# Kernel tuning notes

Hardware: AMD Instinct MI355X
Metric: run time of the kernel (lower is better)

Reference implementation:

```python
import jax, jax.numpy as jnp
import numpy as np

S = 30.0
M = 0.5
EPS = 1e-07


def setup_inputs() -> dict:
    key = jax.random.key(0)
    k1, k2, k3 = jax.random.split(key, 3)
    B, D, C = 1024, 512, 100000
    embeddings = jax.random.normal(k1, (B, D), dtype=jnp.float32)
    # xavier_uniform for weight [C, D]
    limit = float(np.sqrt(6.0 / (C + D)))
    weight = jax.random.uniform(k2, (C, D), dtype=jnp.float32, minval=-limit, maxval=limit)
    labels = jax.random.randint(k3, (B,), 0, C, dtype=jnp.int64)
    return {"embeddings": embeddings, "weight": weight, "labels": labels}


def _l2norm(x, axis=-1):
    # matches F.normalize(p=2, eps=1e-12)
    n = jnp.linalg.norm(x, axis=axis, keepdims=True)
    return x / jnp.maximum(n, 1e-12)


def reference(embeddings, weight, labels):
    # cosine: [B, C] = normalized embeddings @ normalized weight^T
    cosine = _l2norm(embeddings) @ _l2norm(weight).T
    B = cosine.shape[0]
    rows = jnp.arange(B)
    # margin transform only on the target logit per row (same math as
    # one_hot combine: cos(acos(clamp(c)) + m) at the label column)
    tgt = cosine[rows, labels]
    theta = jnp.arccos(jnp.clip(tgt, -1.0 + EPS, 1.0 - EPS))
    target_logit = jnp.cos(theta + M)
    output = cosine.at[rows, labels].set(target_logit)
    return output * S
```

## Files before the change

### kernel.cpp

```cpp
#include <hip/hip_runtime.h>
#include <hip/hip_bf16.h>

typedef __attribute__((ext_vector_type(8))) short bf16x8;
typedef __attribute__((ext_vector_type(4))) float f32x4;

#define B_ROWS 1024
#define C_COLS 100000
#define K_DIM  512
#define SCALE_S 30.0f
#define MARGIN_M 0.5f
#define EPS_C 1e-7f

#define BM 256
#define BN 256
#define BK 64
#define NKT (K_DIM / BK)

__device__ __forceinline__ void gload_lds16(const __hip_bfloat16* g, __hip_bfloat16* l) {
    __builtin_amdgcn_global_load_lds((const __attribute__((address_space(1))) void*)g,
                                     (__attribute__((address_space(3))) void*)l,
                                     16, 0, 0);
}

__device__ __forceinline__ void barrier_fenced() {
    asm volatile("" ::: "memory");
    __builtin_amdgcn_s_barrier();
    asm volatile("" ::: "memory");
}

__global__ __launch_bounds__(256) void l2norm_bf16_rows(const float* __restrict__ in,
                                                        __hip_bfloat16* __restrict__ out,
                                                        int nrows) {
    int wid  = (int)((blockIdx.x * blockDim.x + threadIdx.x) >> 6);
    int lane = threadIdx.x & 63;
    if (wid >= nrows) return;
    const float4* rp = (const float4*)(in + (size_t)wid * K_DIM);
    float4 v0 = rp[lane];
    float4 v1 = rp[lane + 64];
    float ss = v0.x * v0.x + v0.y * v0.y + v0.z * v0.z + v0.w * v0.w
             + v1.x * v1.x + v1.y * v1.y + v1.z * v1.z + v1.w * v1.w;
#pragma unroll
    for (int off = 32; off > 0; off >>= 1) ss += __shfl_xor(ss, off, 64);
    float scale = 1.0f / fmaxf(sqrtf(ss), 1e-12f);
    union { __hip_bfloat16 h[4]; int2 q; } a, b;
    a.h[0] = __float2bfloat16(v0.x * scale);
    a.h[1] = __float2bfloat16(v0.y * scale);
    a.h[2] = __float2bfloat16(v0.z * scale);
    a.h[3] = __float2bfloat16(v0.w * scale);
    b.h[0] = __float2bfloat16(v1.x * scale);
    b.h[1] = __float2bfloat16(v1.y * scale);
    b.h[2] = __float2bfloat16(v1.z * scale);
    b.h[3] = __float2bfloat16(v1.w * scale);
    int2* op = (int2*)(out + (size_t)wid * K_DIM);
    op[lane]      = a.q;
    op[lane + 64] = b.q;
}

__global__ __launch_bounds__(512, 2) void arcface_gemm(
        const __hip_bfloat16* __restrict__ A,
        const __hip_bfloat16* __restrict__ W,
        float* __restrict__ out) {
    __shared__ __hip_bfloat16 sA[2 * 2 * 256 * 32];
    __shared__ __hip_bfloat16 sB[2 * 2 * 256 * 32];

    const int nwg = (int)gridDim.x;
    const int q8 = nwg >> 3, r8 = nwg & 7;
    const int xcd = (int)blockIdx.x & 7, ii = (int)blockIdx.x >> 3;
    const int wg = (xcd < r8 ? xcd * (q8 + 1) : r8 * (q8 + 1) + (xcd - r8) * q8) + ii;
    const int mt = wg & 3, nt = wg >> 2;
    const long m0 = (long)mt * BM;
    const long n0 = (long)nt * BN;

    const int tid  = (int)threadIdx.x;
    const int lane = tid & 63;
    const int w    = tid >> 6;
    const int wm   = w >> 2;
    const int wn   = w & 3;
    const int lidx = lane & 15, lk = lane >> 4;

    const int srow  = tid >> 2;
    const int sslot = (tid & 3) ^ (srow & 3);

#define STAGE_A(buf, kh, kt) do {                                                   \
        gload_lds16(A + (m0 + srow) * K_DIM + (kt) * BK + (kh) * 32 + sslot * 8,    \
                    &sA[((((buf) * 2 + (kh)) * 256) * 32) + (0 * 512 + tid) * 8]);  \
        gload_lds16(A + (m0 + 128 + srow) * K_DIM + (kt) * BK + (kh) * 32 + sslot * 8, \
                    &sA[((((buf) * 2 + (kh)) * 256) * 32) + (1 * 512 + tid) * 8]);  \
    } while (0)

#define STAGE_B(buf, kh, kt) do {                                                   \
        long r0 = n0 + srow;       if (r0 >= C_COLS) r0 = C_COLS - 1;               \
        long r1 = n0 + 128 + srow; if (r1 >= C_COLS) r1 = C_COLS - 1;               \
        gload_lds16(W + r0 * K_DIM + (kt) * BK + (kh) * 32 + sslot * 8,             \
                    &sB[((((buf) * 2 + (kh)) * 256) * 32) + (0 * 512 + tid) * 8]);  \
        gload_lds16(W + r1 * K_DIM + (kt) * BK + (kh) * 32 + sslot * 8,             \
                    &sB[((((buf) * 2 + (kh)) * 256) * 32) + (1 * 512 + tid) * 8]);  \
    } while (0)

#define LDA(dst, c, kh, mh) do {                                                    \
        _Pragma("unroll")                                                           \
        for (int i = 0; i < 4; ++i) {                                               \
            int row = wm * 128 + (mh) * 64 + i * 16 + lidx;                         \
            dst[i] = *(const bf16x8*)&sA[(((c) * 2 + (kh)) * 256 + row) * 32        \
                                         + ((lk ^ (lidx & 3)) * 8)];                \
        }                                                                           \
    } while (0)

#define LDB(dst, c, kh) do {                                                        \
        _Pragma("unroll")                                                           \
        for (int n = 0; n < 4; ++n) {                                               \
            int row = wn * 64 + n * 16 + lidx;                                      \
            dst[n] = *(const bf16x8*)&sB[(((c) * 2 + (kh)) * 256 + row) * 32        \
                                         + ((lk ^ (lidx & 3)) * 8)];                \
        }                                                                           \
    } while (0)

#define MFMA16(mh, av_, bv_) do {                                                   \
        __builtin_amdgcn_s_setprio(1);                                              \
        _Pragma("unroll")                                                           \
        for (int m = 0; m < 4; ++m)                                                 \
            _Pragma("unroll")                                                       \
            for (int n = 0; n < 4; ++n)                                             \
                acc[(mh) * 4 + m][n] = __builtin_amdgcn_mfma_f32_16x16x32_bf16(     \
                    av_[m], bv_[n], acc[(mh) * 4 + m][n], 0, 0, 0);                 \
        __builtin_amdgcn_s_setprio(0);                                              \
    } while (0)

#define WAIT_LGKM0() do { asm volatile("s_waitcnt lgkmcnt(0)" ::: "memory"); \
                          __builtin_amdgcn_sched_barrier(0); } while (0)
#define WAIT_VM4()   asm volatile("s_waitcnt vmcnt(4)" ::: "memory")
#define WAIT_VM0()   asm volatile("s_waitcnt vmcnt(0)" ::: "memory")

    f32x4 acc[8][4];
#pragma unroll
    for (int m = 0; m < 8; ++m)
#pragma unroll
        for (int n = 0; n < 4; ++n) acc[m][n] = (f32x4){0.f, 0.f, 0.f, 0.f};

    STAGE_A(0, 0, 0); STAGE_B(0, 0, 0);
    STAGE_A(0, 1, 0); STAGE_B(0, 1, 0);
    WAIT_VM4();
    barrier_fenced();

    bf16x8 av[4], bv[4];
    for (int t = 0; t < NKT - 1; ++t) {
        const int c = t & 1, nb = c ^ 1;
        LDA(av, c, 0, 0); LDB(bv, c, 0);
        STAGE_A(nb, 0, t + 1);
        barrier_fenced(); WAIT_LGKM0();
        MFMA16(0, av, bv);
        barrier_fenced();
        LDA(av, c, 0, 1);
        STAGE_B(nb, 0, t + 1);
        barrier_fenced(); WAIT_LGKM0();
        MFMA16(1, av, bv);
        WAIT_VM4();
        barrier_fenced();
        LDA(av, c, 1, 0); LDB(bv, c, 1);
        STAGE_A(nb, 1, t + 1);
        barrier_fenced(); WAIT_LGKM0();
        MFMA16(0, av, bv);
        barrier_fenced();
        LDA(av, c, 1, 1);
        STAGE_B(nb, 1, t + 1);
        barrier_fenced(); WAIT_LGKM0();
        MFMA16(1, av, bv);
        WAIT_VM4();
        barrier_fenced();
    }
    {
        const int c = (NKT - 1) & 1;
        LDA(av, c, 0, 0); LDB(bv, c, 0);
        barrier_fenced(); WAIT_LGKM0();
        MFMA16(0, av, bv);
        barrier_fenced();
        LDA(av, c, 0, 1);
        barrier_fenced(); WAIT_LGKM0();
        MFMA16(1, av, bv);
        WAIT_VM0();
        barrier_fenced();
        LDA(av, c, 1, 0); LDB(bv, c, 1);
        barrier_fenced(); WAIT_LGKM0();
        MFMA16(0, av, bv);
        barrier_fenced();
        LDA(av, c, 1, 1);
        barrier_fenced(); WAIT_LGKM0();
        MFMA16(1, av, bv);
    }

    const long colb = n0 + wn * 64 + lidx;
#pragma unroll
    for (int mf = 0; mf < 8; ++mf) {
        long rowb = m0 + wm * 128 + mf * 16 + lk * 4;
#pragma unroll
        for (int nf = 0; nf < 4; ++nf) {
            long gc = colb + nf * 16;
            if (gc < C_COLS) {
#pragma unroll
                for (int j = 0; j < 4; ++j)
                    out[(rowb + j) * (long)C_COLS + gc] = acc[mf][nf][j] * SCALE_S;
            }
        }
    }
#undef STAGE_A
#undef STAGE_B
#undef LDA
#undef LDB
#undef MFMA16
#undef WAIT_LGKM0
#undef WAIT_VM4
#undef WAIT_VM0
}

__global__ void margin_fixup(float* __restrict__ out, const int* __restrict__ labels,
                             int nrows) {
    int b = blockIdx.x * blockDim.x + threadIdx.x;
    if (b >= nrows) return;
    int lab = labels[b];
    size_t idx = (size_t)b * C_COLS + (size_t)lab;
    float c = out[idx] * (1.0f / SCALE_S);
    c = fminf(fmaxf(c, -1.0f + EPS_C), 1.0f - EPS_C);
    float t = acosf(c) + MARGIN_M;
    out[idx] = cosf(t) * SCALE_S;
}

extern "C" void kernel_launch(void* const* d_in, const int* in_sizes, int n_in,
                              void* d_out, int out_size, void* d_ws, size_t ws_size,
                              hipStream_t stream) {
    const float* emb = (const float*)d_in[0];
    const float* wgt = (const float*)d_in[1];
    const int* labels = (const int*)d_in[2];
    float* out = (float*)d_out;

    __hip_bfloat16* embb = (__hip_bfloat16*)d_ws;
    __hip_bfloat16* wgtb = (__hip_bfloat16*)((char*)d_ws + (size_t)B_ROWS * K_DIM * 2);

    l2norm_bf16_rows<<<B_ROWS / 4, 256, 0, stream>>>(emb, embb, B_ROWS);
    l2norm_bf16_rows<<<C_COLS / 4, 256, 0, stream>>>(wgt, wgtb, C_COLS);

    const int ntiles = (C_COLS + BN - 1) / BN;
    arcface_gemm<<<4 * ntiles, 512, 0, stream>>>(embb, wgtb, out);

    margin_fixup<<<(B_ROWS + 255) / 256, 256, 0, stream>>>(out, labels, B_ROWS);
}
```

Before: 703.6 us.

## Make GEMM persistent with XCD-strided tiles, cross-tile prefetch, and vectorized transposed stores

Replaces the one-workgroup-per-tile grid with a persistent grid of 256 workgroups. Each workgroup loops over tiles strided by 32 within its XCD's column group and prefetches the next tile's first K-slab during the current tile's epilogue. The MFMA operands are swapped so each lane holds four consecutive columns, which allows float4 stores instead of scalar strided stores. The aim is to cut launch and tail overhead, overlap loads with the output write, and widen store transactions. In exchange it adds loop bookkeeping and may load-balance less evenly across workgroups.

```diff
diff --git a/kernel.cpp b/kernel.cpp
--- a/kernel.cpp
+++ b/kernel.cpp
@@ -15,6 +15,7 @@
 #define BN 256
 #define BK 64
 #define NKT (K_DIM / BK)
+#define N_TILES ((C_COLS + BN - 1) / BN)
 
 __device__ __forceinline__ void gload_lds16(const __hip_bfloat16* g, __hip_bfloat16* l) {
     __builtin_amdgcn_global_load_lds((const __attribute__((address_space(1))) void*)g,
@@ -63,13 +64,10 @@
     __shared__ __hip_bfloat16 sA[2 * 2 * 256 * 32];
     __shared__ __hip_bfloat16 sB[2 * 2 * 256 * 32];
 
-    const int nwg = (int)gridDim.x;
-    const int q8 = nwg >> 3, r8 = nwg & 7;
-    const int xcd = (int)blockIdx.x & 7, ii = (int)blockIdx.x >> 3;
-    const int wg = (xcd < r8 ? xcd * (q8 + 1) : r8 * (q8 + 1) + (xcd - r8) * q8) + ii;
-    const int mt = wg & 3, nt = wg >> 2;
-    const long m0 = (long)mt * BM;
-    const long n0 = (long)nt * BN;
+    const int x = (int)blockIdx.x & 7;
+    const int s = (int)blockIdx.x >> 3;
+    const int cnt = (x < (N_TILES & 7)) ? (N_TILES / 8 + 1) : (N_TILES / 8);
+    const int tot = 4 * cnt;
 
     const int tid  = (int)threadIdx.x;
     const int lane = tid & 63;
@@ -80,6 +78,9 @@
 
     const int srow  = tid >> 2;
     const int sslot = (tid & 3) ^ (srow & 3);
+
+#define TILE_MN(j) do { m0 = (long)((j) & 3) * BM;                                  \
+                        n0 = (long)(x + 8 * ((j) >> 2)) * BN; } while (0)
 
 #define STAGE_A(buf, kh, kt) do {                                                   \
         gload_lds16(A + (m0 + srow) * K_DIM + (kt) * BK + (kh) * 32 + sslot * 8,    \
@@ -97,6 +98,9 @@
                     &sB[((((buf) * 2 + (kh)) * 256) * 32) + (1 * 512 + tid) * 8]);  \
     } while (0)
 
+#define STAGE_FULL() do { STAGE_A(0, 0, 0); STAGE_B(0, 0, 0);                       \
+                          STAGE_A(0, 1, 0); STAGE_B(0, 1, 0); } while (0)
+
 #define LDA(dst, c, kh, mh) do {                                                    \
         _Pragma("unroll")                                                           \
         for (int i = 0; i < 4; ++i) {                                               \
@@ -122,7 +126,7 @@
             _Pragma("unroll")                                                       \
             for (int n = 0; n < 4; ++n)                                             \
                 acc[(mh) * 4 + m][n] = __builtin_amdgcn_mfma_f32_16x16x32_bf16(     \
-                    av_[m], bv_[n], acc[(mh) * 4 + m][n], 0, 0, 0);                 \
+                    bv_[n], av_[m], acc[(mh) * 4 + m][n], 0, 0, 0);                 \
         __builtin_amdgcn_s_setprio(0);                                              \
     } while (0)
 
@@ -132,78 +136,91 @@
 #define WAIT_VM0()   asm volatile("s_waitcnt vmcnt(0)" ::: "memory")
 
     f32x4 acc[8][4];
-#pragma unroll
-    for (int m = 0; m < 8; ++m)
-#pragma unroll
-        for (int n = 0; n < 4; ++n) acc[m][n] = (f32x4){0.f, 0.f, 0.f, 0.f};
-
-    STAGE_A(0, 0, 0); STAGE_B(0, 0, 0);
-    STAGE_A(0, 1, 0); STAGE_B(0, 1, 0);
-    WAIT_VM4();
-    barrier_fenced();
-
     bf16x8 av[4], bv[4];
-    for (int t = 0; t < NKT - 1; ++t) {
-        const int c = t & 1, nb = c ^ 1;
-        LDA(av, c, 0, 0); LDB(bv, c, 0);
-        STAGE_A(nb, 0, t + 1);
-        barrier_fenced(); WAIT_LGKM0();
-        MFMA16(0, av, bv);
-        barrier_fenced();
-        LDA(av, c, 0, 1);
-        STAGE_B(nb, 0, t + 1);
-        barrier_fenced(); WAIT_LGKM0();
-        MFMA16(1, av, bv);
+    long m0, n0;
+
+    TILE_MN(s);
+    STAGE_FULL();
+
+    for (int j = s; j < tot; j += 32) {
         WAIT_VM4();
         barrier_fenced();
-        LDA(av, c, 1, 0); LDB(bv, c, 1);
-        STAGE_A(nb, 1, t + 1);
-        barrier_fenced(); WAIT_LGKM0();
-        MFMA16(0, av, bv);
-        barrier_fenced();
-        LDA(av, c, 1, 1);
-        STAGE_B(nb, 1, t + 1);
-        barrier_fenced(); WAIT_LGKM0();
-        MFMA16(1, av, bv);
-        WAIT_VM4();
-        barrier_fenced();
+#pragma unroll
+        for (int m = 0; m < 8; ++m)
+#pragma unroll
+            for (int n = 0; n < 4; ++n) acc[m][n] = (f32x4){0.f, 0.f, 0.f, 0.f};
+
+        for (int t = 0; t < NKT - 1; ++t) {
+            const int c = t & 1, nb = c ^ 1;
+            LDA(av, c, 0, 0); LDB(bv, c, 0);
+            STAGE_A(nb, 0, t + 1);
+            barrier_fenced(); WAIT_LGKM0();
+            MFMA16(0, av, bv);
+            barrier_fenced();
+            LDA(av, c, 0, 1);
+            STAGE_B(nb, 0, t + 1);
+            barrier_fenced(); WAIT_LGKM0();
+            MFMA16(1, av, bv);
+            WAIT_VM4();
+            barrier_fenced();
+            LDA(av, c, 1, 0); LDB(bv, c, 1);
+            STAGE_A(nb, 1, t + 1);
+            barrier_fenced(); WAIT_LGKM0();
+            MFMA16(0, av, bv);
+            barrier_fenced();
+            LDA(av, c, 1, 1);
+            STAGE_B(nb, 1, t + 1);
+            barrier_fenced(); WAIT_LGKM0();
+            MFMA16(1, av, bv);
+            WAIT_VM4();
+            barrier_fenced();
+        }
+        {
+            const int c = (NKT - 1) & 1;
+            LDA(av, c, 0, 0); LDB(bv, c, 0);
+            barrier_fenced(); WAIT_LGKM0();
+            MFMA16(0, av, bv);
+            barrier_fenced();
+            LDA(av, c, 0, 1);
+            barrier_fenced(); WAIT_LGKM0();
+            MFMA16(1, av, bv);
+            WAIT_VM0();
+            barrier_fenced();
+            LDA(av, c, 1, 0); LDB(bv, c, 1);
+            barrier_fenced(); WAIT_LGKM0();
+            MFMA16(0, av, bv);
+            barrier_fenced();
+            LDA(av, c, 1, 1);
+            barrier_fenced(); WAIT_LGKM0();
+            MFMA16(1, av, bv);
+        }
+
+        {
+            const long cb = n0 + wn * 64 + lk * 4;
+#pragma unroll
+            for (int mf = 0; mf < 8; ++mf) {
+                float* orow = out + (m0 + wm * 128 + mf * 16 + lidx) * (long)C_COLS;
+#pragma unroll
+                for (int nf = 0; nf < 4; ++nf) {
+                    long c0 = cb + nf * 16;
+                    if (c0 < C_COLS) {
+                        float4 st = { acc[mf][nf][0] * SCALE_S, acc[mf][nf][1] * SCALE_S,
+                                      acc[mf][nf][2] * SCALE_S, acc[mf][nf][3] * SCALE_S };
+                        *(float4*)(orow + c0) = st;
+                    }
+                }
+            }
+        }
+
+        if (j + 32 < tot) {
+            TILE_MN(j + 32);
+            STAGE_FULL();
+        }
     }
-    {
-        const int c = (NKT - 1) & 1;
-        LDA(av, c, 0, 0); LDB(bv, c, 0);
-        barrier_fenced(); WAIT_LGKM0();
-        MFMA16(0, av, bv);
-        barrier_fenced();
-        LDA(av, c, 0, 1);
-        barrier_fenced(); WAIT_LGKM0();
-        MFMA16(1, av, bv);
-        WAIT_VM0();
-        barrier_fenced();
-        LDA(av, c, 1, 0); LDB(bv, c, 1);
-        barrier_fenced(); WAIT_LGKM0();
-        MFMA16(0, av, bv);
-        barrier_fenced();
-        LDA(av, c, 1, 1);
-        barrier_fenced(); WAIT_LGKM0();
-        MFMA16(1, av, bv);
-    }
-
-    const long colb = n0 + wn * 64 + lidx;
-#pragma unroll
-    for (int mf = 0; mf < 8; ++mf) {
-        long rowb = m0 + wm * 128 + mf * 16 + lk * 4;
-#pragma unroll
-        for (int nf = 0; nf < 4; ++nf) {
-            long gc = colb + nf * 16;
-            if (gc < C_COLS) {
-#pragma unroll
-                for (int j = 0; j < 4; ++j)
-                    out[(rowb + j) * (long)C_COLS + gc] = acc[mf][nf][j] * SCALE_S;
-            }
-        }
-    }
+#undef TILE_MN
 #undef STAGE_A
 #undef STAGE_B
+#undef STAGE_FULL
 #undef LDA
 #undef LDB
 #undef MFMA16
@@ -238,8 +255,7 @@
     l2norm_bf16_rows<<<B_ROWS / 4, 256, 0, stream>>>(emb, embb, B_ROWS);
     l2norm_bf16_rows<<<C_COLS / 4, 256, 0, stream>>>(wgt, wgtb, C_COLS);
 
-    const int ntiles = (C_COLS + BN - 1) / BN;
-    arcface_gemm<<<4 * ntiles, 512, 0, stream>>>(embb, wgtb, out);
+    arcface_gemm<<<256, 512, 0, stream>>>(embb, wgtb, out);
 
     margin_fixup<<<(B_ROWS + 255) / 256, 256, 0, stream>>>(out, labels, B_ROWS);
 }
```

Result: slower. 724.8 us (+3.0%).
